# Optimization experiments

Hardware: AMD Instinct MI355X
Metric: run time of the kernel (lower is better)

## Reference

```python
import jax, jax.numpy as jnp
import numpy as np

N = 8192       # tokens
D = 1024       # input_dim
H = 1024       # hidden_dim
E = 8          # num_experts
K = 2          # top-k


def setup_inputs() -> dict:
    key = jax.random.key(0)
    ks = jax.random.split(key, 7)
    s_in = 1.0 / np.sqrt(D)
    s_h = 1.0 / np.sqrt(H)
    return {
        "x": jax.random.normal(ks[0], (N, D), dtype=jnp.float32),
        "W1": jax.random.uniform(ks[1], (E, D, H), jnp.float32, -s_in, s_in),
        "b1": jax.random.uniform(ks[2], (E, H), jnp.float32, -s_in, s_in),
        "W2": jax.random.uniform(ks[3], (E, H, H), jnp.float32, -s_h, s_h),
        "b2": jax.random.uniform(ks[4], (E, H), jnp.float32, -s_h, s_h),
        "Wg": jax.random.uniform(ks[5], (E, D), jnp.float32, -s_in, s_in),
        "bg": jax.random.uniform(ks[6], (E,), jnp.float32, -s_in, s_in),
    }


def reference(x, W1, b1, W2, b2, Wg, bg):
    # Gate: logits [N, E] -> top-k values/indices -> softmax over the k values
    logits = x @ Wg.T + bg
    topk_vals, topk_idx = jax.lax.top_k(logits, K)          # [N, K]
    gates = jax.nn.softmax(topk_vals, axis=1)               # [N, K]

    # Experts (dropout is identity in eval): two Linear+ReLU per expert
    h1 = jax.nn.relu(jnp.einsum('nd,edh->neh', x, W1) + b1[None])   # [N, E, H]
    h2 = jax.nn.relu(jnp.einsum('neh,ehf->nef', h1, W2) + b2[None]) # [N, E, H]

    # Gather each token's top-k expert outputs and combine with gate weights
    sel = jnp.take_along_axis(h2, topk_idx[:, :, None], axis=1)     # [N, K, H]
    return jnp.sum(gates[:, :, None] * sel, axis=1)                  # [N, H]
```

## Files before the change

### kernel.cpp

```cpp
#include <hip/hip_runtime.h>
#include <stdint.h>

#define N_TOK   8192
#define DIMK    1024
#define NEXP    8
#define PADROWS 17408

typedef __attribute__((ext_vector_type(8))) short short8;
typedef __attribute__((ext_vector_type(4))) float f32x4;
typedef unsigned short u16;

__device__ __forceinline__ u16 f2bf(float f) {
  uint32_t u = __builtin_bit_cast(uint32_t, f);
  u += 0x7fffu + ((u >> 16) & 1u);
  return (u16)(u >> 16);
}

__device__ __forceinline__ void load16_lds(const void* g, void* l) {
  __builtin_amdgcn_global_load_lds(
      (const __attribute__((address_space(1))) void*)g,
      (__attribute__((address_space(3))) void*)l, 16, 0, 0);
}

#define OFF_W1T   0u
#define OFF_W2T   16777216u
#define OFF_XP    33554432u
#define OFF_H1    69206016u
#define OFF_GIDX  104857600u
#define OFF_GVAL  104923136u
#define OFF_PTOK  104988672u
#define OFF_PGATE 105058304u
#define OFF_CTRL  105127936u

__global__ void convw_kernel(const float* __restrict__ W1, const float* __restrict__ W2,
                             u16* __restrict__ W1T, u16* __restrict__ W2T) {
  __shared__ u16 tile[64][65];
  int b = (int)blockIdx.x;
  const float* src = W1; u16* dst = W1T;
  if (b >= 2048) { src = W2; dst = W2T; b -= 2048; }
  const int e  = b >> 8;
  const int t  = b & 255;
  const int k0 = (t >> 4) << 6;
  const int n0 = (t & 15) << 6;
  const int tid = (int)threadIdx.x;
  const int r  = tid >> 2;
  const int c4 = (tid & 3) << 4;
  const float4* s = (const float4*)(src + ((size_t)e << 20) +
                                    ((size_t)(k0 + r) << 10) + n0 + c4);
#pragma unroll
  for (int j = 0; j < 4; ++j) {
    float4 v = s[j];
    tile[r][c4 + 4 * j + 0] = f2bf(v.x);
    tile[r][c4 + 4 * j + 1] = f2bf(v.y);
    tile[r][c4 + 4 * j + 2] = f2bf(v.z);
    tile[r][c4 + 4 * j + 3] = f2bf(v.w);
  }
  __syncthreads();
  const int on = tid >> 2;
  const int ok = (tid & 3) << 4;
  u16* d = dst + ((size_t)e << 20) + ((size_t)(n0 + on) << 10) + k0 + ok;
  short8 v0, v1;
#pragma unroll
  for (int j = 0; j < 8; ++j) {
    v0[j] = (short)tile[ok + j][on];
    v1[j] = (short)tile[ok + 8 + j][on];
  }
  *(short8*)d = v0;
  *(short8*)(d + 8) = v1;
}

__global__ void gate_kernel(const float* __restrict__ x, const float* __restrict__ Wg,
                            const float* __restrict__ bg, int* __restrict__ gidx,
                            float* __restrict__ gval, int* __restrict__ counts) {
  __shared__ int hist[NEXP];
  const int tid = (int)threadIdx.x;
  if (tid < NEXP) hist[tid] = 0;
  __syncthreads();
  const int n = (int)blockIdx.x * 4 + (tid >> 6);
  const int lane = tid & 63;
  float acc[NEXP];
#pragma unroll
  for (int e = 0; e < NEXP; ++e) acc[e] = 0.f;
  const float4* xr = (const float4*)(x + ((size_t)n << 10));
#pragma unroll
  for (int j = 0; j < 4; ++j) {
    float4 xv = xr[j * 64 + lane];
#pragma unroll
    for (int e = 0; e < NEXP; ++e) {
      float4 wv = ((const float4*)(Wg + ((size_t)e << 10)))[j * 64 + lane];
      acc[e] += xv.x * wv.x + xv.y * wv.y + xv.z * wv.z + xv.w * wv.w;
    }
  }
#pragma unroll
  for (int e = 0; e < NEXP; ++e)
#pragma unroll
    for (int off = 32; off; off >>= 1) acc[e] += __shfl_xor(acc[e], off, 64);
  if (lane == 0) {
    float lg[NEXP];
#pragma unroll
    for (int e = 0; e < NEXP; ++e) lg[e] = acc[e] + bg[e];
    int e0 = 0; float v0 = lg[0];
#pragma unroll
    for (int e = 1; e < NEXP; ++e) if (lg[e] > v0) { v0 = lg[e]; e0 = e; }
    int e1 = -1; float v1 = -1e30f;
#pragma unroll
    for (int e = 0; e < NEXP; ++e) if (e != e0 && lg[e] > v1) { v1 = lg[e]; e1 = e; }
    float t = expf(v1 - v0);
    float g0 = 1.f / (1.f + t);
    gidx[2 * n] = e0; gidx[2 * n + 1] = e1;
    gval[2 * n] = g0; gval[2 * n + 1] = t * g0;
    atomicAdd(&hist[e0], 1); atomicAdd(&hist[e1], 1);
  }
  __syncthreads();
  if (tid < NEXP && hist[tid]) atomicAdd(&counts[tid], hist[tid]);
}

__global__ void scan_kernel(const int* __restrict__ counts, int* __restrict__ poff) {
  if (threadIdx.x == 0) {
    int off = 0; poff[0] = 0;
    for (int e = 0; e < NEXP; ++e) { off += ((counts[e] + 127) >> 7) << 7; poff[e + 1] = off; }
  }
}

__global__ void scatter_kernel(const int* __restrict__ gidx, const float* __restrict__ gval,
                               const int* __restrict__ poff, int* __restrict__ cursor,
                               int* __restrict__ ptok, float* __restrict__ pgate) {
  const int n = (int)blockIdx.x * 256 + (int)threadIdx.x;
#pragma unroll
  for (int k = 0; k < 2; ++k) {
    const int e = gidx[2 * n + k];
    const int p = poff[e] + atomicAdd(&cursor[e], 1);
    ptok[p] = n;
    pgate[p] = gval[2 * n + k];
  }
}

__global__ void gather_kernel(const float* __restrict__ x, const int* __restrict__ ptok,
                              u16* __restrict__ xp) {
  const int p = (int)blockIdx.x * 4 + ((int)threadIdx.x >> 6);
  const int lane = (int)threadIdx.x & 63;
  const int tok = ptok[p];
  const float4* src = (const float4*)(x + ((size_t)tok << 10));
  ushort4* dst = (ushort4*)(xp + ((size_t)p << 10));
#pragma unroll
  for (int j = 0; j < 4; ++j) {
    float4 v = src[j * 64 + lane];
    ushort4 o; o.x = f2bf(v.x); o.y = f2bf(v.y); o.z = f2bf(v.z); o.w = f2bf(v.w);
    dst[j * 64 + lane] = o;
  }
}

template <int PASS>
__global__ __launch_bounds__(256, 2)
void gemm_kernel(const u16* __restrict__ A, const u16* __restrict__ WT,
                 const float* __restrict__ bias, const int* __restrict__ poff,
                 const int* __restrict__ ptok, const float* __restrict__ pgate,
                 u16* __restrict__ Hout, float* __restrict__ Out,
                 int* __restrict__ qhead) {
  __shared__ u16 As[2][128 * 64];
  __shared__ u16 Bs[2][128 * 64];
  __shared__ int tokS[128];
  __shared__ float gateS[128];
  __shared__ int tileS;

  const int tid = (int)threadIdx.x;
  const int lane = tid & 63;
  const int wid = tid >> 6;
  const int wm = (wid >> 1) * 64;
  const int wn = (wid & 1) * 64;
  const int r_in = lane >> 3;
  const int s_phys = lane & 7;

  const int total = (poff[NEXP] >> 7) * 8;

  for (;;) {
    if (tid == 0) tileS = atomicAdd(qhead, 1);
    __syncthreads();
    const int tile = tileS;
    if (tile >= total) break;
    const int rt = tile >> 3;
    const int ct = tile & 7;
    const int row0 = rt * 128;
    int e = 0;
    while (row0 >= poff[e + 1]) ++e;

    const u16* Ab = A + ((size_t)row0 << 10);
    const u16* Bb = WT + ((size_t)e << 20) + ((size_t)(ct * 128) << 10);

    if (PASS == 2 && tid < 128) {
      tokS[tid] = ptok[row0 + tid];
      gateS[tid] = pgate[row0 + tid];
    }

    f32x4 acc[4][4] = {};

#define STAGE(BUF, K0)                                                         \
  {                                                                            \
    _Pragma("unroll")                                                          \
    for (int i = 0; i < 4; ++i) {                                              \
      const int chunk = wid * 4 + i;                                           \
      const int row = chunk * 8 + r_in;                                        \
      const int slotL = s_phys ^ (row & 7);                                    \
      const size_t goff = ((size_t)row << 10) + (size_t)((K0) + slotL * 8);    \
      load16_lds(Ab + goff, &As[BUF][chunk * 512]);                            \
      load16_lds(Bb + goff, &Bs[BUF][chunk * 512]);                            \
    }                                                                          \
  }

#define COMPUTE(BUF)                                                           \
  {                                                                            \
    _Pragma("unroll")                                                          \
    for (int kk = 0; kk < 2; ++kk) {                                           \
      short8 af[4], bf_[4];                                                    \
      const int kslot = kk * 4 + (lane >> 4);                                  \
      _Pragma("unroll")                                                        \
      for (int mi = 0; mi < 4; ++mi) {                                         \
        const int m = wm + mi * 16 + (lane & 15);                              \
        af[mi] = *(const short8*)((const char*)&As[BUF][0] + m * 128 +         \
                                  ((kslot ^ (m & 7)) << 4));                   \
      }                                                                        \
      _Pragma("unroll")                                                        \
      for (int ni = 0; ni < 4; ++ni) {                                         \
        const int n = wn + ni * 16 + (lane & 15);                              \
        bf_[ni] = *(const short8*)((const char*)&Bs[BUF][0] + n * 128 +        \
                                   ((kslot ^ (n & 7)) << 4));                  \
      }                                                                        \
      _Pragma("unroll")                                                        \
      for (int mi = 0; mi < 4; ++mi)                                           \
        _Pragma("unroll")                                                      \
        for (int ni = 0; ni < 4; ++ni)                                         \
          acc[mi][ni] = __builtin_amdgcn_mfma_f32_16x16x32_bf16(               \
              af[mi], bf_[ni], acc[mi][ni], 0, 0, 0);                          \
    }                                                                          \
  }

    STAGE(0, 0)
#pragma unroll
    for (int t = 0; t < 16; ++t) {
      if (t < 15) {
        STAGE((t + 1) & 1, (t + 1) * 64)
        asm volatile("s_waitcnt vmcnt(8)" ::: "memory");
      } else {
        asm volatile("s_waitcnt vmcnt(0)" ::: "memory");
      }
      __builtin_amdgcn_s_barrier();
      COMPUTE(t & 1)
      asm volatile("s_waitcnt lgkmcnt(0)" ::: "memory");
      __builtin_amdgcn_s_barrier();
    }

    const float* bb = bias + (e << 10) + ct * 128;
    const int cbase = lane & 15;
    const int rbase = (lane >> 4) * 4;
#pragma unroll
    for (int ni = 0; ni < 4; ++ni) {
      const int col = wn + ni * 16 + cbase;
      const float bv = bb[col];
#pragma unroll
      for (int mi = 0; mi < 4; ++mi) {
        const int mb = wm + mi * 16 + rbase;
#pragma unroll
        for (int j = 0; j < 4; ++j) {
          float v = fmaxf(acc[mi][ni][j] + bv, 0.0f);
          if (PASS == 1) {
            Hout[((size_t)(row0 + mb + j) << 10) + (size_t)(ct * 128 + col)] = f2bf(v);
          } else {
            const int m = mb + j;
            unsafeAtomicAdd(Out + ((size_t)tokS[m] << 10) + (size_t)(ct * 128 + col),
                            v * gateS[m]);
          }
        }
      }
    }
#undef STAGE
#undef COMPUTE
  }
}

extern "C" void kernel_launch(void* const* d_in, const int* in_sizes, int n_in,
                              void* d_out, int out_size, void* d_ws, size_t ws_size,
                              hipStream_t stream) {
  (void)in_sizes; (void)n_in; (void)ws_size;
  const float* x  = (const float*)d_in[0];
  const float* W1 = (const float*)d_in[1];
  const float* b1 = (const float*)d_in[2];
  const float* W2 = (const float*)d_in[3];
  const float* b2 = (const float*)d_in[4];
  const float* Wg = (const float*)d_in[5];
  const float* bg = (const float*)d_in[6];
  float* out = (float*)d_out;
  char* ws = (char*)d_ws;

  u16*   W1T   = (u16*)(ws + OFF_W1T);
  u16*   W2T   = (u16*)(ws + OFF_W2T);
  u16*   xp    = (u16*)(ws + OFF_XP);
  u16*   h1    = (u16*)(ws + OFF_H1);
  int*   gidx  = (int*)(ws + OFF_GIDX);
  float* gval  = (float*)(ws + OFF_GVAL);
  int*   ptok  = (int*)(ws + OFF_PTOK);
  float* pgate = (float*)(ws + OFF_PGATE);
  int*   counts = (int*)(ws + OFF_CTRL);
  int*   cursor = counts + 8;
  int*   poff   = counts + 16;
  int*   qh1    = counts + 25;
  int*   qh2    = counts + 26;

  hipMemsetAsync(d_out, 0, (size_t)out_size * 4, stream);
  hipMemsetAsync(ws + OFF_PTOK, 0, 139392, stream);

  convw_kernel<<<4096, 256, 0, stream>>>(W1, W2, W1T, W2T);
  gate_kernel<<<N_TOK / 4, 256, 0, stream>>>(x, Wg, bg, gidx, gval, counts);
  scan_kernel<<<1, 64, 0, stream>>>(counts, poff);
  scatter_kernel<<<N_TOK / 256, 256, 0, stream>>>(gidx, gval, poff, cursor, ptok, pgate);
  gather_kernel<<<PADROWS / 4, 256, 0, stream>>>(x, ptok, xp);
  gemm_kernel<1><<<512, 256, 0, stream>>>(xp, W1T, b1, poff, ptok, pgate, h1, nullptr, qh1);
  gemm_kernel<2><<<512, 256, 0, stream>>>(h1, W2T, b2, poff, ptok, pgate, nullptr, out, qh2);
}
```

Measured before the change: 323.7 us.

## Enlarge GEMM tiles to 256x256 with 512 threads and static grid

Grows the expert GEMM tile from 128x128 to 256x256, with 8 waves each computing 128x64, and pads expert segments to multiples of 256 rows. The persistent atomic work queue is replaced by a static grid of 288 blocks, with early exit for unused row tiles. The explicit vmcnt waits and barriers around the double-buffered LDS are replaced by plain __syncthreads. The larger tile is meant to raise operand reuse and cut global traffic, at the cost of more padding rows, higher register and LDS pressure (128 KB LDS per block), and fewer blocks for load balance.

```diff
diff --git a/kernel.cpp b/kernel.cpp
--- a/kernel.cpp
+++ b/kernel.cpp
@@ -4,7 +4,7 @@
 #define N_TOK   8192
 #define DIMK    1024
 #define NEXP    8
-#define PADROWS 17408
+#define PADROWS 18432
 
 typedef __attribute__((ext_vector_type(8))) short short8;
 typedef __attribute__((ext_vector_type(4))) float f32x4;
@@ -25,12 +25,12 @@
 #define OFF_W1T   0u
 #define OFF_W2T   16777216u
 #define OFF_XP    33554432u
-#define OFF_H1    69206016u
-#define OFF_GIDX  104857600u
-#define OFF_GVAL  104923136u
-#define OFF_PTOK  104988672u
-#define OFF_PGATE 105058304u
-#define OFF_CTRL  105127936u
+#define OFF_H1    71303168u
+#define OFF_GIDX  109051904u
+#define OFF_GVAL  109117440u
+#define OFF_PTOK  109182976u
+#define OFF_PGATE 109256704u
+#define OFF_CTRL  109330432u
 
 __global__ void convw_kernel(const float* __restrict__ W1, const float* __restrict__ W2,
                              u16* __restrict__ W1T, u16* __restrict__ W2T) {
@@ -118,7 +118,7 @@
 __global__ void scan_kernel(const int* __restrict__ counts, int* __restrict__ poff) {
   if (threadIdx.x == 0) {
     int off = 0; poff[0] = 0;
-    for (int e = 0; e < NEXP; ++e) { off += ((counts[e] + 127) >> 7) << 7; poff[e + 1] = off; }
+    for (int e = 0; e < NEXP; ++e) { off += ((counts[e] + 255) >> 8) << 8; poff[e + 1] = off; }
   }
 }
 
@@ -151,59 +151,53 @@
 }
 
 template <int PASS>
-__global__ __launch_bounds__(256, 2)
+__global__ __launch_bounds__(512, 2)
 void gemm_kernel(const u16* __restrict__ A, const u16* __restrict__ WT,
                  const float* __restrict__ bias, const int* __restrict__ poff,
                  const int* __restrict__ ptok, const float* __restrict__ pgate,
-                 u16* __restrict__ Hout, float* __restrict__ Out,
-                 int* __restrict__ qhead) {
-  __shared__ u16 As[2][128 * 64];
-  __shared__ u16 Bs[2][128 * 64];
-  __shared__ int tokS[128];
-  __shared__ float gateS[128];
-  __shared__ int tileS;
+                 u16* __restrict__ Hout, float* __restrict__ Out) {
+  __shared__ u16 As[2][256 * 64];
+  __shared__ u16 Bs[2][256 * 64];
+  __shared__ int tokS[256];
+  __shared__ float gateS[256];
+
+  const int nrt = poff[NEXP] >> 8;
+  const int rt = (int)blockIdx.x >> 2;
+  if (rt >= nrt) return;
+  const int ct = (int)blockIdx.x & 3;
 
   const int tid = (int)threadIdx.x;
   const int lane = tid & 63;
   const int wid = tid >> 6;
-  const int wm = (wid >> 1) * 64;
-  const int wn = (wid & 1) * 64;
+  const int wm = (wid >> 2) * 128;
+  const int wn = (wid & 3) * 64;
   const int r_in = lane >> 3;
   const int s_phys = lane & 7;
 
-  const int total = (poff[NEXP] >> 7) * 8;
-
-  for (;;) {
-    if (tid == 0) tileS = atomicAdd(qhead, 1);
-    __syncthreads();
-    const int tile = tileS;
-    if (tile >= total) break;
-    const int rt = tile >> 3;
-    const int ct = tile & 7;
-    const int row0 = rt * 128;
-    int e = 0;
-    while (row0 >= poff[e + 1]) ++e;
-
-    const u16* Ab = A + ((size_t)row0 << 10);
-    const u16* Bb = WT + ((size_t)e << 20) + ((size_t)(ct * 128) << 10);
-
-    if (PASS == 2 && tid < 128) {
-      tokS[tid] = ptok[row0 + tid];
-      gateS[tid] = pgate[row0 + tid];
-    }
-
-    f32x4 acc[4][4] = {};
+  const int row0 = rt << 8;
+  int e = 0;
+  while (row0 >= poff[e + 1]) ++e;
+
+  const u16* Ab = A + ((size_t)row0 << 10);
+  const u16* Wb = WT + ((size_t)e << 20) + ((size_t)(ct << 8) << 10);
+
+  if (PASS == 2 && tid < 256) {
+    tokS[tid] = ptok[row0 + tid];
+    gateS[tid] = pgate[row0 + tid];
+  }
+
+  f32x4 acc[8][4] = {};
 
 #define STAGE(BUF, K0)                                                         \
   {                                                                            \
     _Pragma("unroll")                                                          \
     for (int i = 0; i < 4; ++i) {                                              \
-      const int chunk = wid * 4 + i;                                           \
+      const int chunk = wid * 4 + i;           \
       const int row = chunk * 8 + r_in;                                        \
       const int slotL = s_phys ^ (row & 7);                                    \
       const size_t goff = ((size_t)row << 10) + (size_t)((K0) + slotL * 8);    \
       load16_lds(Ab + goff, &As[BUF][chunk * 512]);                            \
-      load16_lds(Bb + goff, &Bs[BUF][chunk * 512]);                            \
+      load16_lds(Wb + goff, &Bs[BUF][chunk * 512]);                            \
     }                                                                          \
   }
 
@@ -211,10 +205,10 @@
   {                                                                            \
     _Pragma("unroll")                                                          \
     for (int kk = 0; kk < 2; ++kk) {                                           \
-      short8 af[4], bf_[4];                                                    \
+      short8 af[8], bf_[4];                                                    \
       const int kslot = kk * 4 + (lane >> 4);                                  \
       _Pragma("unroll")                                                        \
-      for (int mi = 0; mi < 4; ++mi) {                                         \
+      for (int mi = 0; mi < 8; ++mi) {                                         \
         const int m = wm + mi * 16 + (lane & 15);                              \
         af[mi] = *(const short8*)((const char*)&As[BUF][0] + m * 128 +         \
                                   ((kslot ^ (m & 7)) << 4));                   \
@@ -226,7 +220,7 @@
                                    ((kslot ^ (n & 7)) << 4));                  \
       }                                                                        \
       _Pragma("unroll")                                                        \
-      for (int mi = 0; mi < 4; ++mi)                                           \
+      for (int mi = 0; mi < 8; ++mi)                                           \
         _Pragma("unroll")                                                      \
         for (int ni = 0; ni < 4; ++ni)                                         \
           acc[mi][ni] = __builtin_amdgcn_mfma_f32_16x16x32_bf16(               \
@@ -234,47 +228,40 @@
     }                                                                          \
   }
 
-    STAGE(0, 0)
-#pragma unroll
-    for (int t = 0; t < 16; ++t) {
-      if (t < 15) {
-        STAGE((t + 1) & 1, (t + 1) * 64)
-        asm volatile("s_waitcnt vmcnt(8)" ::: "memory");
-      } else {
-        asm volatile("s_waitcnt vmcnt(0)" ::: "memory");
-      }
-      __builtin_amdgcn_s_barrier();
-      COMPUTE(t & 1)
-      asm volatile("s_waitcnt lgkmcnt(0)" ::: "memory");
-      __builtin_amdgcn_s_barrier();
-    }
-
-    const float* bb = bias + (e << 10) + ct * 128;
-    const int cbase = lane & 15;
-    const int rbase = (lane >> 4) * 4;
-#pragma unroll
-    for (int ni = 0; ni < 4; ++ni) {
-      const int col = wn + ni * 16 + cbase;
-      const float bv = bb[col];
-#pragma unroll
-      for (int mi = 0; mi < 4; ++mi) {
-        const int mb = wm + mi * 16 + rbase;
-#pragma unroll
-        for (int j = 0; j < 4; ++j) {
-          float v = fmaxf(acc[mi][ni][j] + bv, 0.0f);
-          if (PASS == 1) {
-            Hout[((size_t)(row0 + mb + j) << 10) + (size_t)(ct * 128 + col)] = f2bf(v);
-          } else {
-            const int m = mb + j;
-            unsafeAtomicAdd(Out + ((size_t)tokS[m] << 10) + (size_t)(ct * 128 + col),
-                            v * gateS[m]);
-          }
+  STAGE(0, 0)
+  __syncthreads();
+#pragma unroll 2
+  for (int kt = 0; kt < 16; ++kt) {
+    if (kt < 15) STAGE((kt + 1) & 1, (kt + 1) * 64)
+    COMPUTE(kt & 1)
+    __syncthreads();
+  }
+
+  const float* bb = bias + (e << 10) + (ct << 8);
+  const int cbase = lane & 15;
+  const int rbase = (lane >> 4) * 4;
+#pragma unroll
+  for (int ni = 0; ni < 4; ++ni) {
+    const int col = wn + ni * 16 + cbase;
+    const float bv = bb[col];
+#pragma unroll
+    for (int mi = 0; mi < 8; ++mi) {
+      const int mb = wm + mi * 16 + rbase;
+#pragma unroll
+      for (int j = 0; j < 4; ++j) {
+        float v = fmaxf(acc[mi][ni][j] + bv, 0.0f);
+        if (PASS == 1) {
+          Hout[((size_t)(row0 + mb + j) << 10) + (size_t)((ct << 8) + col)] = f2bf(v);
+        } else {
+          const int m = mb + j;
+          unsafeAtomicAdd(Out + ((size_t)tokS[m] << 10) + (size_t)((ct << 8) + col),
+                          v * gateS[m]);
         }
       }
     }
+  }
 #undef STAGE
 #undef COMPUTE
-  }
 }
 
 extern "C" void kernel_launch(void* const* d_in, const int* in_sizes, int n_in,
@@ -302,17 +289,15 @@
   int*   counts = (int*)(ws + OFF_CTRL);
   int*   cursor = counts + 8;
   int*   poff   = counts + 16;
-  int*   qh1    = counts + 25;
-  int*   qh2    = counts + 26;
 
   hipMemsetAsync(d_out, 0, (size_t)out_size * 4, stream);
-  hipMemsetAsync(ws + OFF_PTOK, 0, 139392, stream);
+  hipMemsetAsync(ws + OFF_PTOK, 0, 147968, stream);
 
   convw_kernel<<<4096, 256, 0, stream>>>(W1, W2, W1T, W2T);
   gate_kernel<<<N_TOK / 4, 256, 0, stream>>>(x, Wg, bg, gidx, gval, counts);
   scan_kernel<<<1, 64, 0, stream>>>(counts, poff);
   scatter_kernel<<<N_TOK / 256, 256, 0, stream>>>(gidx, gval, poff, cursor, ptok, pgate);
   gather_kernel<<<PADROWS / 4, 256, 0, stream>>>(x, ptok, xp);
-  gemm_kernel<1><<<512, 256, 0, stream>>>(xp, W1T, b1, poff, ptok, pgate, h1, nullptr, qh1);
-  gemm_kernel<2><<<512, 256, 0, stream>>>(h1, W2T, b2, poff, ptok, pgate, nullptr, out, qh2);
-}
+  gemm_kernel<1><<<288, 512, 0, stream>>>(xp, W1T, b1, poff, ptok, pgate, h1, nullptr);
+  gemm_kernel<2><<<288, 512, 0, stream>>>(h1, W2T, b2, poff, ptok, pgate, nullptr, out);
+}
```

Result: slower. 421.4 us (+30.2%).

## Deepen GEMM pipeline to 4-stage K=32 buffers with new LDS swizzle and grid size

Applied to the files above, without the earlier changes.

Splits each K step into 32-wide slices held in four LDS buffers, prefetching three stages ahead instead of one, which hides more global-load latency. The LDS layout and XOR swizzle change to match the narrower 64-byte rows. The grid also grows from 512 persistent blocks to one block per possible tile (136*8). In exchange there are twice as many barriers per tile, and each sync covers less MFMA work.

```diff
diff --git a/kernel.cpp b/kernel.cpp
--- a/kernel.cpp
+++ b/kernel.cpp
@@ -5,6 +5,7 @@
 #define DIMK    1024
 #define NEXP    8
 #define PADROWS 17408
+#define MAXRT   136
 
 typedef __attribute__((ext_vector_type(8))) short short8;
 typedef __attribute__((ext_vector_type(4))) float f32x4;
@@ -157,8 +158,8 @@
                  const int* __restrict__ ptok, const float* __restrict__ pgate,
                  u16* __restrict__ Hout, float* __restrict__ Out,
                  int* __restrict__ qhead) {
-  __shared__ u16 As[2][128 * 64];
-  __shared__ u16 Bs[2][128 * 64];
+  __shared__ u16 As[4][128 * 32];
+  __shared__ u16 Bs[4][128 * 32];
   __shared__ int tokS[128];
   __shared__ float gateS[128];
   __shared__ int tileS;
@@ -168,8 +169,9 @@
   const int wid = tid >> 6;
   const int wm = (wid >> 1) * 64;
   const int wn = (wid & 1) * 64;
-  const int r_in = lane >> 3;
-  const int s_phys = lane & 7;
+  const int st_row = lane >> 2;
+  const int st_slot = ((lane & 3) ^ ((lane >> 3) & 3)) * 8;
+  const int rdslot = (((lane >> 4) ^ ((lane >> 1) & 3)) * 8);
 
   const int total = (poff[NEXP] >> 7) * 8;
 
@@ -194,14 +196,13 @@
 
     f32x4 acc[4][4] = {};
 
-#define STAGE(BUF, K0)                                                         \
+#define STAGE(BUF, T)                                                          \
   {                                                                            \
     _Pragma("unroll")                                                          \
-    for (int i = 0; i < 4; ++i) {                                              \
-      const int chunk = wid * 4 + i;                                           \
-      const int row = chunk * 8 + r_in;                                        \
-      const int slotL = s_phys ^ (row & 7);                                    \
-      const size_t goff = ((size_t)row << 10) + (size_t)((K0) + slotL * 8);    \
+    for (int j = 0; j < 2; ++j) {                                              \
+      const int chunk = wid * 2 + j;                   \
+      const int row = chunk * 16 + st_row;                                     \
+      const size_t goff = ((size_t)row << 10) + (size_t)((T) * 32 + st_slot);  \
       load16_lds(Ab + goff, &As[BUF][chunk * 512]);                            \
       load16_lds(Bb + goff, &Bs[BUF][chunk * 512]);                            \
     }                                                                          \
@@ -209,42 +210,40 @@
 
 #define COMPUTE(BUF)                                                           \
   {                                                                            \
+    short8 af[4], bf_[4];                                                      \
     _Pragma("unroll")                                                          \
-    for (int kk = 0; kk < 2; ++kk) {                                           \
-      short8 af[4], bf_[4];                                                    \
-      const int kslot = kk * 4 + (lane >> 4);                                  \
+    for (int mi = 0; mi < 4; ++mi) {                                           \
+      const int m = wm + mi * 16 + (lane & 15);                                \
+      af[mi] = *(const short8*)(&As[BUF][m * 32 + rdslot]);                    \
+    }                                                                          \
+    _Pragma("unroll")                                                          \
+    for (int ni = 0; ni < 4; ++ni) {                                           \
+      const int n = wn + ni * 16 + (lane & 15);                                \
+      bf_[ni] = *(const short8*)(&Bs[BUF][n * 32 + rdslot]);                   \
+    }                                                                          \
+    _Pragma("unroll")                                                          \
+    for (int mi = 0; mi < 4; ++mi)                                             \
       _Pragma("unroll")                                                        \
-      for (int mi = 0; mi < 4; ++mi) {                                         \
-        const int m = wm + mi * 16 + (lane & 15);                              \
-        af[mi] = *(const short8*)((const char*)&As[BUF][0] + m * 128 +         \
-                                  ((kslot ^ (m & 7)) << 4));                   \
-      }                                                                        \
-      _Pragma("unroll")                                                        \
-      for (int ni = 0; ni < 4; ++ni) {                                         \
-        const int n = wn + ni * 16 + (lane & 15);                              \
-        bf_[ni] = *(const short8*)((const char*)&Bs[BUF][0] + n * 128 +        \
-                                   ((kslot ^ (n & 7)) << 4));                  \
-      }                                                                        \
-      _Pragma("unroll")                                                        \
-      for (int mi = 0; mi < 4; ++mi)                                           \
-        _Pragma("unroll")                                                      \
-        for (int ni = 0; ni < 4; ++ni)                                         \
-          acc[mi][ni] = __builtin_amdgcn_mfma_f32_16x16x32_bf16(               \
-              af[mi], bf_[ni], acc[mi][ni], 0, 0, 0);                          \
-    }                                                                          \
-  }
-
-    STAGE(0, 0)
-#pragma unroll
-    for (int t = 0; t < 16; ++t) {
-      if (t < 15) {
-        STAGE((t + 1) & 1, (t + 1) * 64)
+      for (int ni = 0; ni < 4; ++ni)                                           \
+        acc[mi][ni] = __builtin_amdgcn_mfma_f32_16x16x32_bf16(                 \
+            af[mi], bf_[ni], acc[mi][ni], 0, 0, 0);                            \
+  }
+
+    STAGE(0, 0) STAGE(1, 1) STAGE(2, 2)
+#pragma unroll
+    for (int t = 0; t < 32; ++t) {
+      if (t < 29) {
+        STAGE((t + 3) & 3, t + 3)
+        asm volatile("s_waitcnt vmcnt(12)" ::: "memory");
+      } else if (t == 29) {
         asm volatile("s_waitcnt vmcnt(8)" ::: "memory");
+      } else if (t == 30) {
+        asm volatile("s_waitcnt vmcnt(4)" ::: "memory");
       } else {
         asm volatile("s_waitcnt vmcnt(0)" ::: "memory");
       }
       __builtin_amdgcn_s_barrier();
-      COMPUTE(t & 1)
+      COMPUTE(t & 3)
       asm volatile("s_waitcnt lgkmcnt(0)" ::: "memory");
       __builtin_amdgcn_s_barrier();
     }
@@ -313,6 +312,6 @@
   scan_kernel<<<1, 64, 0, stream>>>(counts, poff);
   scatter_kernel<<<N_TOK / 256, 256, 0, stream>>>(gidx, gval, poff, cursor, ptok, pgate);
   gather_kernel<<<PADROWS / 4, 256, 0, stream>>>(x, ptok, xp);
-  gemm_kernel<1><<<512, 256, 0, stream>>>(xp, W1T, b1, poff, ptok, pgate, h1, nullptr, qh1);
-  gemm_kernel<2><<<512, 256, 0, stream>>>(h1, W2T, b2, poff, ptok, pgate, nullptr, out, qh2);
-}
+  gemm_kernel<1><<<MAXRT * 8, 256, 0, stream>>>(xp, W1T, b1, poff, ptok, pgate, h1, nullptr, qh1);
+  gemm_kernel<2><<<MAXRT * 8, 256, 0, stream>>>(h1, W2T, b2, poff, ptok, pgate, nullptr, out, qh2);
+}
```

After: 339.5 us. 1.05x slower.

## Prefetch next tile's first K-stage during epilogue and stage PASS1 stores through LDS

Applied to the files above, without the earlier changes.

The persistent GEMM loop now fetches the next tile index mid-loop and issues the next tile's first K-slice loads before running the current tile's epilogue. Global memory latency at tile boundaries should then overlap with compute and the epilogue. For pass 1, results are written to an LDS scratch area that aliases the second buffer, then stored to global memory as coalesced 16-byte rows instead of scattered 2-byte stores. The cost is more complex synchronisation, double-buffered token and gate arrays, and a risk of hazards on the reused LDS buffers.

```diff
diff --git a/kernel.cpp b/kernel.cpp
--- a/kernel.cpp
+++ b/kernel.cpp
@@ -5,6 +5,7 @@
 #define DIMK    1024
 #define NEXP    8
 #define PADROWS 17408
+#define MAXRT   136
 
 typedef __attribute__((ext_vector_type(8))) short short8;
 typedef __attribute__((ext_vector_type(4))) float f32x4;
@@ -157,11 +158,16 @@
                  const int* __restrict__ ptok, const float* __restrict__ pgate,
                  u16* __restrict__ Hout, float* __restrict__ Out,
                  int* __restrict__ qhead) {
-  __shared__ u16 As[2][128 * 64];
-  __shared__ u16 Bs[2][128 * 64];
-  __shared__ int tokS[128];
-  __shared__ float gateS[128];
-  __shared__ int tileS;
+  __shared__ u16 LDS[33792];
+  __shared__ int tokS[2][128];
+  __shared__ float gateS[2][128];
+  __shared__ int tileShare;
+
+  u16* const As0 = &LDS[0];
+  u16* const Bs0 = &LDS[8192];
+  u16* const As1 = &LDS[16384];
+  u16* const Bs1 = &LDS[24576];
+  u16* const scratch = &LDS[16384];
 
   const int tid = (int)threadIdx.x;
   const int lane = tid & 63;
@@ -170,44 +176,25 @@
   const int wn = (wid & 1) * 64;
   const int r_in = lane >> 3;
   const int s_phys = lane & 7;
+  const int cbase = lane & 15;
+  const int rbase = (lane >> 4) * 4;
 
   const int total = (poff[NEXP] >> 7) * 8;
 
-  for (;;) {
-    if (tid == 0) tileS = atomicAdd(qhead, 1);
-    __syncthreads();
-    const int tile = tileS;
-    if (tile >= total) break;
-    const int rt = tile >> 3;
-    const int ct = tile & 7;
-    const int row0 = rt * 128;
-    int e = 0;
-    while (row0 >= poff[e + 1]) ++e;
-
-    const u16* Ab = A + ((size_t)row0 << 10);
-    const u16* Bb = WT + ((size_t)e << 20) + ((size_t)(ct * 128) << 10);
-
-    if (PASS == 2 && tid < 128) {
-      tokS[tid] = ptok[row0 + tid];
-      gateS[tid] = pgate[row0 + tid];
-    }
-
-    f32x4 acc[4][4] = {};
-
-#define STAGE(BUF, K0)                                                         \
+#define STAGE(ADST, BDST, ABASE, BBASE, K0)                                    \
   {                                                                            \
     _Pragma("unroll")                                                          \
-    for (int i = 0; i < 4; ++i) {                                              \
-      const int chunk = wid * 4 + i;                                           \
-      const int row = chunk * 8 + r_in;                                        \
-      const int slotL = s_phys ^ (row & 7);                                    \
-      const size_t goff = ((size_t)row << 10) + (size_t)((K0) + slotL * 8);    \
-      load16_lds(Ab + goff, &As[BUF][chunk * 512]);                            \
-      load16_lds(Bb + goff, &Bs[BUF][chunk * 512]);                            \
+    for (int i_ = 0; i_ < 4; ++i_) {                                           \
+      const int chunk_ = wid * 4 + i_;                                         \
+      const int row_ = chunk_ * 8 + r_in;                                      \
+      const int slotL_ = s_phys ^ (row_ & 7);                                  \
+      const size_t goff_ = ((size_t)row_ << 10) + (size_t)((K0) + slotL_ * 8); \
+      load16_lds((ABASE) + goff_, (ADST) + chunk_ * 512);                      \
+      load16_lds((BBASE) + goff_, (BDST) + chunk_ * 512);                      \
     }                                                                          \
   }
 
-#define COMPUTE(BUF)                                                           \
+#define COMPUTE(ASRC, BSRC)                                                    \
   {                                                                            \
     _Pragma("unroll")                                                          \
     for (int kk = 0; kk < 2; ++kk) {                                           \
@@ -215,14 +202,14 @@
       const int kslot = kk * 4 + (lane >> 4);                                  \
       _Pragma("unroll")                                                        \
       for (int mi = 0; mi < 4; ++mi) {                                         \
-        const int m = wm + mi * 16 + (lane & 15);                              \
-        af[mi] = *(const short8*)((const char*)&As[BUF][0] + m * 128 +         \
+        const int m = wm + mi * 16 + cbase;                                    \
+        af[mi] = *(const short8*)((const char*)(ASRC) + m * 128 +              \
                                   ((kslot ^ (m & 7)) << 4));                   \
       }                                                                        \
       _Pragma("unroll")                                                        \
       for (int ni = 0; ni < 4; ++ni) {                                         \
-        const int n = wn + ni * 16 + (lane & 15);                              \
-        bf_[ni] = *(const short8*)((const char*)&Bs[BUF][0] + n * 128 +        \
+        const int n = wn + ni * 16 + cbase;                                    \
+        bf_[ni] = *(const short8*)((const char*)(BSRC) + n * 128 +             \
                                    ((kslot ^ (n & 7)) << 4));                  \
       }                                                                        \
       _Pragma("unroll")                                                        \
@@ -234,47 +221,121 @@
     }                                                                          \
   }
 
-    STAGE(0, 0)
-#pragma unroll
-    for (int t = 0; t < 16; ++t) {
-      if (t < 15) {
-        STAGE((t + 1) & 1, (t + 1) * 64)
-        asm volatile("s_waitcnt vmcnt(8)" ::: "memory");
-      } else {
-        asm volatile("s_waitcnt vmcnt(0)" ::: "memory");
-      }
+  if (tid == 0) tileShare = atomicAdd(qhead, 1);
+  __syncthreads();
+  int tile = tileShare;
+  if (tile >= total) return;
+  int par = 0;
+  int ct = tile & 7;
+  int row0 = (tile >> 3) << 7;
+  int e = 0;
+  while (row0 >= poff[e + 1]) ++e;
+  const u16* Ab = A + ((size_t)row0 << 10);
+  const u16* Bb = WT + ((size_t)e << 20) + ((size_t)(ct * 128) << 10);
+  if (PASS == 2) {
+    const int q = tid & 127;
+    tokS[0][q] = ptok[row0 + q];
+    gateS[0][q] = pgate[row0 + q];
+  }
+  STAGE(As0, Bs0, Ab, Bb, 0)
+  asm volatile("s_waitcnt vmcnt(0)" ::: "memory");
+  __builtin_amdgcn_s_barrier();
+
+  int nextT = 0;
+  for (;;) {
+    f32x4 acc[4][4] = {};
+
+    STAGE(As1, Bs1, Ab, Bb, 64)
+    asm volatile("s_waitcnt vmcnt(16)" ::: "memory");
+    __builtin_amdgcn_s_barrier();
+    COMPUTE(As0, Bs0)
+    asm volatile("s_waitcnt lgkmcnt(0)" ::: "memory");
+    __builtin_amdgcn_s_barrier();
+
+#pragma unroll
+    for (int t = 1; t < 15; ++t) {
+      if (t == 8) { if (tid == 0) nextT = atomicAdd(qhead, 1); }
+      if (t & 1) { STAGE(As0, Bs0, Ab, Bb, (t + 1) * 64) }
+      else       { STAGE(As1, Bs1, Ab, Bb, (t + 1) * 64) }
+      asm volatile("s_waitcnt vmcnt(8)" ::: "memory");
       __builtin_amdgcn_s_barrier();
-      COMPUTE(t & 1)
+      if (t & 1) { COMPUTE(As1, Bs1) }
+      else       { COMPUTE(As0, Bs0) }
+      if (t == 14) { if (tid == 0) tileShare = nextT; }
       asm volatile("s_waitcnt lgkmcnt(0)" ::: "memory");
       __builtin_amdgcn_s_barrier();
     }
 
+    const int nt = tileShare;
+    const bool valid = nt < total;
+    const int tU = valid ? nt : tile;
+    const int ctN = tU & 7;
+    const int row0N = (tU >> 3) << 7;
+    int eN = 0;
+    while (row0N >= poff[eN + 1]) ++eN;
+    const u16* AbN = A + ((size_t)row0N << 10);
+    const u16* BbN = WT + ((size_t)eN << 20) + ((size_t)(ctN * 128) << 10);
+    if (PASS == 2) {
+      const int q = tid & 127;
+      tokS[par ^ 1][q] = ptok[row0N + q];
+      gateS[par ^ 1][q] = pgate[row0N + q];
+    }
+    STAGE(As0, Bs0, AbN, BbN, 0)
+    asm volatile("s_waitcnt vmcnt(8)" ::: "memory");
+    __builtin_amdgcn_s_barrier();
+    COMPUTE(As1, Bs1)
+    asm volatile("s_waitcnt lgkmcnt(0)" ::: "memory");
+    __builtin_amdgcn_s_barrier();
+
     const float* bb = bias + (e << 10) + ct * 128;
-    const int cbase = lane & 15;
-    const int rbase = (lane >> 4) * 4;
-#pragma unroll
-    for (int ni = 0; ni < 4; ++ni) {
-      const int col = wn + ni * 16 + cbase;
-      const float bv = bb[col];
-#pragma unroll
-      for (int mi = 0; mi < 4; ++mi) {
-        const int mb = wm + mi * 16 + rbase;
-#pragma unroll
-        for (int j = 0; j < 4; ++j) {
-          float v = fmaxf(acc[mi][ni][j] + bv, 0.0f);
-          if (PASS == 1) {
-            Hout[((size_t)(row0 + mb + j) << 10) + (size_t)(ct * 128 + col)] = f2bf(v);
-          } else {
+    if (PASS == 1) {
+#pragma unroll
+      for (int ni = 0; ni < 4; ++ni) {
+        const int col = wn + ni * 16 + cbase;
+        const float bv = bb[col];
+#pragma unroll
+        for (int mi = 0; mi < 4; ++mi) {
+          const int mb = wm + mi * 16 + rbase;
+#pragma unroll
+          for (int j = 0; j < 4; ++j)
+            scratch[(mb + j) * 136 + col] = f2bf(fmaxf(acc[mi][ni][j] + bv, 0.0f));
+        }
+      }
+      asm volatile("s_waitcnt lgkmcnt(0)" ::: "memory");
+      __builtin_amdgcn_s_barrier();
+#pragma unroll
+      for (int q = 0; q < 8; ++q) {
+        const int idx = q * 2048 + tid * 8;
+        const int row = idx >> 7, colq = idx & 127;
+        short8 v = *(const short8*)&scratch[row * 136 + colq];
+        *(short8*)&Hout[((size_t)(row0 + row) << 10) + (size_t)(ct * 128 + colq)] = v;
+      }
+      asm volatile("s_waitcnt lgkmcnt(0)" ::: "memory");
+      __builtin_amdgcn_s_barrier();
+    } else {
+#pragma unroll
+      for (int ni = 0; ni < 4; ++ni) {
+        const int col = wn + ni * 16 + cbase;
+        const float bv = bb[col];
+#pragma unroll
+        for (int mi = 0; mi < 4; ++mi) {
+          const int mb = wm + mi * 16 + rbase;
+#pragma unroll
+          for (int j = 0; j < 4; ++j) {
             const int m = mb + j;
-            unsafeAtomicAdd(Out + ((size_t)tokS[m] << 10) + (size_t)(ct * 128 + col),
-                            v * gateS[m]);
+            float v = fmaxf(acc[mi][ni][j] + bv, 0.0f);
+            unsafeAtomicAdd(Out + ((size_t)tokS[par][m] << 10) + (size_t)(ct * 128 + col),
+                            v * gateS[par][m]);
           }
         }
       }
     }
+
+    if (!valid) break;
+    tile = tU; ct = ctN; row0 = row0N; e = eN; Ab = AbN; Bb = BbN; par ^= 1;
+  }
 #undef STAGE
 #undef COMPUTE
-  }
 }
 
 extern "C" void kernel_launch(void* const* d_in, const int* in_sizes, int n_in,
```

After: 335.5 us. 1.04x slower.
